# Kernel optimization log

Hardware: AMD Instinct MI355X
Metric: run time of the kernel (lower is better)

The kernel has to match this reference:

```python
import jax, jax.numpy as jnp
import numpy as np

EPS = 1e-6
NUM_HEADS = 12


def ln_cf(x, w, b):
    # channels_first LayerNorm over channel dim (ConvNeXt style)
    u = jnp.mean(x, axis=1, keepdims=True)
    s = jnp.mean((x - u) ** 2, axis=1, keepdims=True)
    xn = (x - u) / jnp.sqrt(s + EPS)
    shp = (1, -1) + (1,) * (x.ndim - 2)
    return xn * w.reshape(shp) + b.reshape(shp)


def conv2s2(x, w):
    # Conv3d kernel=2 stride=2 (no bias): exact non-overlapping patch contraction
    b, c, H, W, D = x.shape
    xp = x.reshape(b, c, H // 2, 2, W // 2, 2, D // 2, 2)
    return jnp.einsum('bchkwpdq,ockpq->bohwd', xp, w)


def convt2s2(x, w):
    # ConvTranspose3d kernel=2 stride=2 (torch weight layout [in, out, 2,2,2])
    b, i, H, W, D = x.shape
    o = w.shape[1]
    y = jnp.einsum('bihwd,iokpq->bohkwpdq', x, w)
    return y.reshape(b, o, 2 * H, 2 * W, 2 * D)


def stem(x, w1, g1, b1, w2, g2, b2):
    h = conv2s2(x, w1)
    h = jax.nn.gelu(ln_cf(h, g1, b1), approximate=False)
    h = conv2s2(h, w2)
    return ln_cf(h, g2, b2)


def debed(x, tw1, g, b, tw2, tb2):
    h = convt2s2(x, tw1)
    h = jax.nn.gelu(ln_cf(h, g, b), approximate=False)
    return convt2s2(h, tw2) + tb2.reshape(1, -1, 1, 1, 1)


def rope(x):
    # rotary embedding over full token dim c (pairs (i, i+c/2)), positions 0..L-1
    b, l, c = x.shape
    inv = 1.0 / (10000.0 ** (jnp.arange(0, c, 2, dtype=jnp.float32) / c))
    t = jnp.arange(l, dtype=jnp.float32)
    f = jnp.outer(t, inv)                      # [l, c/2]
    emb = jnp.concatenate([f, f], axis=-1)     # [l, c]
    cos, sin = jnp.cos(emb)[None], jnp.sin(emb)[None]
    rot = jnp.concatenate([-x[..., c // 2:], x[..., :c // 2]], axis=-1)
    return x * cos + rot * sin


def _forward(x, skip, q_w1, q_g1, q_b1, q_w2, q_g2, q_b2,
             k_w1, k_g1, k_b1, k_w2, k_g2, k_b2,
             v_w1, v_g1, v_b1, v_w2, v_g2, v_b2,
             o_tw1, o_g, o_b, o_tw2, o_tb2,
             ns_w, ns_b, nx_w, nx_b, no_w, no_b):
    res = skip
    skip = ln_cf(skip, ns_w, ns_b)
    x = ln_cf(x, nx_w, nx_b)
    q = stem(skip, q_w1, q_g1, q_b1, q_w2, q_g2, q_b2)
    k = stem(x, k_w1, k_g1, k_b1, k_w2, k_g2, k_b2)
    v = stem(x, v_w1, v_g1, v_b1, v_w2, v_g2, v_b2)
    b, c, Hq, Wq, Dq = q.shape
    _, _, Hk, Wk, Dk = k.shape
    q = q.reshape(b, c, -1).transpose(0, 2, 1)   # [b, Lq, c]
    k = k.reshape(b, c, -1).transpose(0, 2, 1)   # [b, Lk, c]
    v = v.reshape(b, c, -1).transpose(0, 2, 1)
    q = rope(q)
    k = rope(k)
    hd = c // NUM_HEADS
    qh = q.reshape(b, -1, NUM_HEADS, hd).transpose(0, 2, 1, 3)  # [b, nh, Lq, hd]
    kh = k.reshape(b, -1, NUM_HEADS, hd).transpose(0, 2, 1, 3)
    vh = v.reshape(b, -1, NUM_HEADS, hd).transpose(0, 2, 1, 3)
    scale = 1.0 / jnp.sqrt(jnp.float32(hd))
    attn = jax.nn.softmax(jnp.einsum('bhqc,bhkc->bhqk', qh, kh) * scale, axis=-1)
    proj = jnp.einsum('bhqk,bhkc->bhqc', attn, vh)              # [b, nh, Lq, hd]
    # rearrange 'b nh l c -> b (c nh) h w d'
    proj = proj.transpose(0, 3, 1, 2).reshape(b, c, Hq, Wq, Dq)
    proj = ln_cf(proj, no_w, no_b)
    out = debed(proj, o_tw1, o_g, o_b, o_tw2, o_tb2)
    return out + res


def setup_inputs() -> dict:
    key = jax.random.key(0)
    ks = iter(jax.random.split(key, 40))
    def nrm(shape, scale):
        return jax.random.normal(next(ks), shape, jnp.float32) * scale
    E, E4, XF, SF = 768, 192, 6, 6
    inp = {
        'x': nrm((2, XF, 48, 48, 48), 1.0),
        'skip': nrm((2, SF, 48, 48, 48), 1.0),
    }
    for p, ic in [('q', SF), ('k', XF), ('v', XF)]:
        inp[p + '_w1'] = nrm((E4, ic, 2, 2, 2), (ic * 8) ** -0.5)
        inp[p + '_g1'] = jnp.ones(E4, jnp.float32)
        inp[p + '_b1'] = jnp.zeros(E4, jnp.float32)
        inp[p + '_w2'] = nrm((E, E4, 2, 2, 2), (E4 * 8) ** -0.5)
        inp[p + '_g2'] = jnp.ones(E, jnp.float32)
        inp[p + '_b2'] = jnp.zeros(E, jnp.float32)
    inp['o_tw1'] = nrm((E, E4, 2, 2, 2), E ** -0.5)
    inp['o_g'] = jnp.ones(E4, jnp.float32)
    inp['o_b'] = jnp.zeros(E4, jnp.float32)
    inp['o_tw2'] = nrm((E4, SF, 2, 2, 2), E4 ** -0.5)
    inp['o_tb2'] = jnp.zeros(SF, jnp.float32)
    inp['ns_w'] = jnp.ones(SF, jnp.float32)
    inp['ns_b'] = jnp.zeros(SF, jnp.float32)
    inp['nx_w'] = jnp.ones(XF, jnp.float32)
    inp['nx_b'] = jnp.zeros(XF, jnp.float32)
    inp['no_w'] = jnp.ones(E, jnp.float32)
    inp['no_b'] = jnp.zeros(E, jnp.float32)
    return inp


def reference(x, skip, q_w1, q_g1, q_b1, q_w2, q_g2, q_b2,
              k_w1, k_g1, k_b1, k_w2, k_g2, k_b2,
              v_w1, v_g1, v_b1, v_w2, v_g2, v_b2,
              o_tw1, o_g, o_b, o_tw2, o_tb2,
              ns_w, ns_b, nx_w, nx_b, no_w, no_b):
    return _forward(x, skip, q_w1, q_g1, q_b1, q_w2, q_g2, q_b2,
                    k_w1, k_g1, k_b1, k_w2, k_g2, k_b2,
                    v_w1, v_g1, v_b1, v_w2, v_g2, v_b2,
                    o_tw1, o_g, o_b, o_tw2, o_tb2,
                    ns_w, ns_b, nx_w, nx_b, no_w, no_b)
```

## Files before the change

### kernel.cpp

```cpp
#include <hip/hip_runtime.h>
#include <math.h>

#define BB_ 2
#define C0 6
#define S0 48
#define V0 (S0*S0*S0)
#define C1 192
#define S1 24
#define V1 (S1*S1*S1)
#define C2 768
#define S2 12
#define LL (S2*S2*S2)
#define NH 12
#define HD 64
#define KDIM (C1*8)
#define MDIM (BB_*LL)

typedef __attribute__((ext_vector_type(8))) short short8;
typedef __attribute__((ext_vector_type(4))) short short4v;
typedef __attribute__((ext_vector_type(4))) float float4v;

static __device__ __forceinline__ float gelu_exact(float x){
  return 0.5f*x*(1.0f+erff(x*0.70710678118654752440f));
}
static __device__ __forceinline__ unsigned short f2bf(float f){
  unsigned int u = __float_as_uint(f);
  unsigned int r = (u + 0x7fffu + ((u>>16)&1u)) >> 16;
  return (unsigned short)r;
}
static __device__ __forceinline__ unsigned int pk_bf16(float a, float b){
#if __has_builtin(__builtin_amdgcn_cvt_pk_bf16_f32)
  typedef __attribute__((ext_vector_type(2))) __bf16 bf2;
  bf2 r = __builtin_amdgcn_cvt_pk_bf16_f32(a,b);
  union { bf2 v; unsigned int u; } cv; cv.v = r;
  return cv.u;
#else
  return (unsigned int)f2bf(a) | ((unsigned int)f2bf(b)<<16);
#endif
}
static __device__ __forceinline__ float bf2f(unsigned short u){
  return __uint_as_float(((unsigned int)u)<<16);
}
static __device__ __forceinline__ void load_lds16(const void* g, void* l){
  __builtin_amdgcn_global_load_lds((const __attribute__((address_space(1))) unsigned int*)g,
      (__attribute__((address_space(3))) unsigned int*)l, 16, 0, 0);
}
static __device__ __forceinline__ float4v mfma32(short8 a, short8 b, float4v c){
  return __builtin_amdgcn_mfma_f32_16x16x32_bf16(a,b,c,0,0,0);
}
static __device__ __forceinline__ float4v mfma16(short4v a, short4v b, float4v c){
#if __has_builtin(__builtin_amdgcn_mfma_f32_16x16x16bf16_1k)
  return __builtin_amdgcn_mfma_f32_16x16x16bf16_1k(a,b,c,0,0,0);
#else
  asm volatile("v_mfma_f32_16x16x16_bf16 %0, %1, %2, %0" : "+v"(c) : "v"(a), "v"(b));
  return c;
#endif
}

__global__ __launch_bounds__(256) void prep_kernel(
    const float* __restrict__ skin, const float* __restrict__ xin,
    const float* __restrict__ nsw, const float* __restrict__ nsb,
    const float* __restrict__ nxw, const float* __restrict__ nxb,
    unsigned short* __restrict__ outS, unsigned short* __restrict__ outX,
    const float* __restrict__ qw2, const float* __restrict__ kw2, const float* __restrict__ vw2,
    const float* __restrict__ tw1, const float* __restrict__ tw2,
    const float* __restrict__ qw1, const float* __restrict__ kw1, const float* __restrict__ vw1,
    unsigned short* __restrict__ w2tq, unsigned short* __restrict__ w2tk,
    unsigned short* __restrict__ w2tv, unsigned short* __restrict__ Btd,
    unsigned short* __restrict__ Bt48,
    unsigned short* __restrict__ w1q, unsigned short* __restrict__ w1k,
    unsigned short* __restrict__ w1v){
  int bx = blockIdx.x;
  if (bx < 1728){
    int z = bx >= 864;
    const float* in = z ? xin : skin;
    const float* w  = z ? nxw : nsw;
    const float* bi = z ? nxb : nsb;
    unsigned short* out = z ? outX : outS;
    int idx = (bx - z*864)*256 + threadIdx.x;
    int b = idx / V0, vox = idx - b*V0;
    const float* p = in + (size_t)b*(C0*V0) + vox;
    float v[C0]; float s=0.f;
#pragma unroll
    for (int c=0;c<C0;c++){ v[c]=p[(size_t)c*V0]; s+=v[c]; }
    float u = s*(1.f/C0);
    float ss=0.f;
#pragma unroll
    for (int c=0;c<C0;c++){ float d=v[c]-u; ss+=d*d; }
    float inv = rsqrtf(ss*(1.f/C0)+1e-6f);
    unsigned short* o = out + (size_t)b*(C0*V0) + vox;
#pragma unroll
    for (int c=0;c<C0;c++) o[(size_t)c*V0] = f2bf((v[c]-u)*inv*w[c]+bi[c]);
    return;
  }
  bx -= 1728;
  if (bx < 13824){
    int z = bx/4608;
    int idx = (bx - z*4608)*256 + threadIdx.x;
    const float* w2 = (z==0)?qw2:((z==1)?kw2:vw2);
    unsigned short* o = (z==0)?w2tq:((z==1)?w2tk:w2tv);
    int oc = idx/KDIM; int r = idx-oc*KDIM; int p = r/C1; int ic = r-p*C1;
    o[idx] = f2bf(w2[(size_t)oc*KDIM + ic*8 + p]);
  } else if (bx < 18432){
    int idx = (bx-13824)*256 + threadIdx.x;
    int n = idx/C2; int p = idx-n*C2;
    int i = ((p&63)*NH) + (p>>6);
    int kpq = n/C1, o2 = n-kpq*C1;
    Btd[idx] = f2bf(tw1[(size_t)i*KDIM + o2*8 + kpq]);
  } else if (bx < 18480){
    int idx = (bx-18432)*256 + threadIdx.x;
    int n = idx/C1; int i = idx-n*C1;
    Bt48[idx] = (n<48) ? f2bf(tw2[(size_t)i*48 + n]) : (unsigned short)0;
  } else {
    int idx = (bx-18480)*256 + threadIdx.x;
    int z = idx / 9216; int r = idx - z*9216;
    const float* w1 = (z==0)?qw1:((z==1)?kw1:vw1);
    unsigned short* o = (z==0)?w1q:((z==1)?w1k:w1v);
    o[r] = f2bf(w1[r]);
  }
}

__global__ __launch_bounds__(256) void conv1_kernel(
    const unsigned short* __restrict__ lnSb, const unsigned short* __restrict__ lnXb,
    const unsigned short* __restrict__ w1bq, const unsigned short* __restrict__ w1bk,
    const unsigned short* __restrict__ w1bv,
    const float* __restrict__ qg1, const float* __restrict__ qb1,
    const float* __restrict__ kg1, const float* __restrict__ kb1,
    const float* __restrict__ vg1, const float* __restrict__ vb1,
    unsigned short* __restrict__ h1q, unsigned short* __restrict__ h1k,
    unsigned short* __restrict__ h1v){
  int z = blockIdx.z;
  const unsigned short* in = (z==0)? lnSb : lnXb;
  const unsigned short* Wb = (z==0)?w1bq:((z==1)?w1bk:w1bv);
  const float* g1 = (z==0)?qg1:((z==1)?kg1:vg1);
  const float* b1 = (z==0)?qb1:((z==1)?kb1:vb1);
  unsigned short* h1p = (z==0)?h1q:((z==1)?h1k:h1v);
  int t = threadIdx.x, w = t>>6, lane = t&63;
  int g = lane>>4, l16 = lane&15;
  int j = blockIdx.x*4 + w;
  int bxh = j/18, mt = j - bxh*18;
  int b = bxh/48; int rem = bxh - b*48; int y = rem>>1, xh = rem&1;
  int xo = mt/3, zo = mt - xo*3;
  int xv = xh*12 + xo*2 + (l16>>3);
  int zv = zo*8 + (l16&7);
  int x2 = 2*xv, z2 = 2*zv, y2 = 2*y;
  const unsigned short* base = in + (size_t)b*C0*V0;
  union { short8 v; unsigned int u[4]; } aA;
  {
    size_t rb = (size_t)g*V0;
    aA.u[0] = *(const unsigned int*)&base[rb + (y2+0)*(S0*S0) + (x2+0)*S0 + z2];
    aA.u[1] = *(const unsigned int*)&base[rb + (y2+0)*(S0*S0) + (x2+1)*S0 + z2];
    aA.u[2] = *(const unsigned int*)&base[rb + (y2+1)*(S0*S0) + (x2+0)*S0 + z2];
    aA.u[3] = *(const unsigned int*)&base[rb + (y2+1)*(S0*S0) + (x2+1)*S0 + z2];
  }
  union { short4v v; unsigned int u[2]; } aB;
  {
    size_t rb = (size_t)(4+(g>>1))*V0 + (y2+(g&1))*(S0*S0);
    aB.u[0] = *(const unsigned int*)&base[rb + (x2+0)*S0 + z2];
    aB.u[1] = *(const unsigned int*)&base[rb + (x2+1)*S0 + z2];
  }
  float4v acc[12];
#pragma unroll
  for (int ot=0; ot<12; ot++){
    short8  wA = *(const short8*)&Wb[(ot*16+l16)*48 + g*8];
    short4v wB = *(const short4v*)&Wb[(ot*16+l16)*48 + 32 + g*4];
    float4v a = {};
    a = mfma32(wA, aA.v, a);
    a = mfma16(wB, aB.v, a);
    acc[ot] = a;
  }
  float s1=0.f, s2=0.f;
#pragma unroll
  for (int ot=0;ot<12;ot++)
#pragma unroll
    for (int reg=0;reg<4;reg++){ float v=acc[ot][reg]; s1+=v; s2+=v*v; }
  s1 += __shfl_xor(s1,16); s1 += __shfl_xor(s1,32);
  s2 += __shfl_xor(s2,16); s2 += __shfl_xor(s2,32);
  float u = s1*(1.f/C1);
  float inv = rsqrtf(s2*(1.f/C1)-u*u+1e-6f);
  int tok = (y>>1)*(S2*S2) + (xv>>1)*S2 + (zv>>1);
  int p8 = (y&1)*4 + (xv&1)*2 + (zv&1);
  unsigned short* hb = h1p + (size_t)(b*LL+tok)*KDIM + p8*C1;
#pragma unroll
  for (int ot=0; ot<12; ot++){
    int oc0 = ot*16 + g*4;
    float4 gg = *(const float4*)&g1[oc0];
    float4 bb = *(const float4*)&b1[oc0];
    float x0 = gelu_exact((acc[ot][0]-u)*inv*gg.x+bb.x);
    float x1 = gelu_exact((acc[ot][1]-u)*inv*gg.y+bb.y);
    float x2e= gelu_exact((acc[ot][2]-u)*inv*gg.z+bb.z);
    float x3 = gelu_exact((acc[ot][3]-u)*inv*gg.w+bb.w);
    uint2 pk; pk.x = pk_bf16(x0,x1); pk.y = pk_bf16(x2e,x3);
    *(uint2*)&hb[oc0] = pk;
  }
}

__global__ __launch_bounds__(256) void gemm_stem_kernel(
    const unsigned short* __restrict__ A0, const unsigned short* __restrict__ A1,
    const unsigned short* __restrict__ A2,
    const unsigned short* __restrict__ B0, const unsigned short* __restrict__ B1,
    const unsigned short* __restrict__ B2,
    unsigned short* __restrict__ Cq, unsigned short* __restrict__ Ck,
    unsigned short* __restrict__ Cv){
  int flat = blockIdx.x;
  int xcd = flat & 7, slot = flat >> 3;
  int tile = xcd*61 + slot;
  if (tile >= 486) return;
  int z = tile/162; int rr = tile - z*162;
  int m0 = (rr/6)*128, n0 = (rr - (rr/6)*6)*128;
  const unsigned short* A = (z==0)?A0:((z==1)?A1:A2);
  const unsigned short* Bt = (z==0)?B0:((z==1)?B1:B2);
  unsigned short* Cp = (z==0)?Cq:((z==1)?Ck:Cv);
  __shared__ __align__(16) unsigned short Al[128*32];
  __shared__ __align__(16) unsigned short Bl[128*32];
  int t=threadIdx.x, w=t>>6, lane=t&63;
  int g=lane>>4, l16=lane&15, r16=lane>>2, c16=lane&3;
  int wm=w>>1, wn=w&1;
  float4v acc[4][4] = {};
  for (int kb=0;kb<KDIM;kb+=32){
    __syncthreads();
#pragma unroll
    for (int cc=0;cc<4;cc++){
      int ch = w*4+cc;
      if (ch<8){
        const unsigned short* gp = A + (size_t)(m0+ch*16+r16)*KDIM + kb + c16*8;
        load_lds16(gp, &Al[ch*512]);
      } else {
        const unsigned short* gp = Bt + (size_t)(n0+(ch-8)*16+r16)*KDIM + kb + c16*8;
        load_lds16(gp, &Bl[(ch-8)*512]);
      }
    }
    __syncthreads();
    short8 af[4], bf[4];
#pragma unroll
    for (int mt=0;mt<4;mt++) af[mt] = *(const short8*)&Al[(wm*64+mt*16+l16)*32 + g*8];
#pragma unroll
    for (int nt=0;nt<4;nt++) bf[nt] = *(const short8*)&Bl[(wn*64+nt*16+l16)*32 + g*8];
#pragma unroll
    for (int mt=0;mt<4;mt++)
#pragma unroll
      for (int nt=0;nt<4;nt++)
        acc[mt][nt] = mfma32(af[mt], bf[nt], acc[mt][nt]);
  }
#pragma unroll
  for (int mt=0;mt<4;mt++){
    int mb = m0 + wm*64 + mt*16 + g*4;
#pragma unroll
    for (int nt=0;nt<4;nt++){
      int col = n0 + wn*64 + nt*16 + l16;
#pragma unroll
      for (int reg=0;reg<4;reg++)
        Cp[(size_t)(mb+reg)*C2 + col] = f2bf(acc[mt][nt][reg]);
    }
  }
}

__global__ __launch_bounds__(256) void gemm_debed_kernel(const unsigned short* __restrict__ A,
    const unsigned short* __restrict__ Bt, unsigned short* __restrict__ C){
  int flat = blockIdx.x;
  int xcd = flat & 7, slot = flat >> 3;
  int tile = xcd*41 + slot;
  if (tile >= 324) return;
  int m0 = (tile/12)*128, n0 = (tile - (tile/12)*12)*128;
  __shared__ __align__(16) unsigned short Al[128*32];
  __shared__ __align__(16) unsigned short Bl[128*32];
  int t=threadIdx.x, w=t>>6, lane=t&63;
  int g=lane>>4, l16=lane&15, r16=lane>>2, c16=lane&3;
  int wm=w>>1, wn=w&1;
  float4v acc[4][4] = {};
  for (int kb=0;kb<C2;kb+=32){
    __syncthreads();
#pragma unroll
    for (int cc=0;cc<4;cc++){
      int ch = w*4+cc;
      if (ch<8){
        const unsigned short* gp = A + (size_t)(m0+ch*16+r16)*C2 + kb + c16*8;
        load_lds16(gp, &Al[ch*512]);
      } else {
        const unsigned short* gp = Bt + (size_t)(n0+(ch-8)*16+r16)*C2 + kb + c16*8;
        load_lds16(gp, &Bl[(ch-8)*512]);
      }
    }
    __syncthreads();
    short8 af[4], bf[4];
#pragma unroll
    for (int mt=0;mt<4;mt++) af[mt] = *(const short8*)&Al[(wm*64+mt*16+l16)*32 + g*8];
#pragma unroll
    for (int nt=0;nt<4;nt++) bf[nt] = *(const short8*)&Bl[(wn*64+nt*16+l16)*32 + g*8];
#pragma unroll
    for (int mt=0;mt<4;mt++)
#pragma unroll
      for (int nt=0;nt<4;nt++)
        acc[mt][nt] = mfma32(af[mt], bf[nt], acc[mt][nt]);
  }
#pragma unroll
  for (int nt=0;nt<4;nt++){
    int n = n0 + wn*64 + nt*16 + l16;
    int kpq = n / C1;
    int o = n - kpq*C1;
#pragma unroll
    for (int mt=0;mt<4;mt++){
      int mb = m0 + wm*64 + mt*16 + g*4;
#pragma unroll
      for (int reg=0;reg<4;reg++){
        int m = mb + reg;
        int b = m / LL; int tok = m - b*LL;
        int h = tok/(S2*S2), ww=(tok/S2)%S2, d=tok%S2;
        int v24 = (2*h+((kpq>>2)&1))*(S1*S1) + (2*ww+((kpq>>1)&1))*S1 + (2*d+(kpq&1));
        C[(size_t)(b*V1+v24)*C1 + o] = f2bf(acc[mt][nt][reg]);
      }
    }
  }
}

__global__ __launch_bounds__(256) void final_kernel(const unsigned short* __restrict__ dh,
    const unsigned short* __restrict__ Bt48, const float* __restrict__ og,
    const float* __restrict__ ob, const float* __restrict__ tb2s,
    const float* __restrict__ skipp, float* __restrict__ out){
  __shared__ __align__(16) unsigned short As[64*200];
  __shared__ __align__(16) unsigned short Bs[64*200];
  int t=threadIdx.x, w=t>>6, lane=t&63;
  int g=lane>>4, l16=lane&15;
  int m0 = blockIdx.x*64;
  for (int n8 = t; n8 < 1536; n8 += 256){
    int n64 = n8/24, kk = (n8 - n64*24)*8;
    uint4 d4 = *(const uint4*)&Bt48[n64*192 + kk];
    *(uint4*)&Bs[n64*200 + kk] = d4;
  }
  float g0=og[lane], g1v=og[lane+64], g2v=og[lane+128];
  float b0=ob[lane], b1v=ob[lane+64], b2v=ob[lane+128];
  for (int rr=0; rr<16; rr++){
    int rl = w*16 + rr;
    const unsigned short* row = dh + (size_t)(m0+rl)*C1;
    float v0=bf2f(row[lane]), v1=bf2f(row[lane+64]), v2=bf2f(row[lane+128]);
    float s1=v0+v1+v2, s2=v0*v0+v1*v1+v2*v2;
#pragma unroll
    for (int off=32;off>0;off>>=1){ s1+=__shfl_xor(s1,off); s2+=__shfl_xor(s2,off); }
    float u=s1*(1.f/C1), inv=rsqrtf(s2*(1.f/C1)-u*u+1e-6f);
    As[rl*200+lane]     = f2bf(gelu_exact((v0-u)*inv*g0+b0));
    As[rl*200+lane+64]  = f2bf(gelu_exact((v1-u)*inv*g1v+b1v));
    As[rl*200+lane+128] = f2bf(gelu_exact((v2-u)*inv*g2v+b2v));
  }
  __syncthreads();
  int wm=w>>1, wn=w&1;
  float4v acc[2][2] = {};
#pragma unroll
  for (int kb=0;kb<192;kb+=32){
    short8 af[2], bf[2];
#pragma unroll
    for (int mt=0;mt<2;mt++) af[mt] = *(const short8*)&As[(wm*32+mt*16+l16)*200 + kb + g*8];
#pragma unroll
    for (int nt=0;nt<2;nt++) bf[nt] = *(const short8*)&Bs[(wn*32+nt*16+l16)*200 + kb + g*8];
#pragma unroll
    for (int mt=0;mt<2;mt++)
#pragma unroll
      for (int nt=0;nt<2;nt++)
        acc[mt][nt] = mfma32(af[mt], bf[nt], acc[mt][nt]);
  }
#pragma unroll
  for (int nt=0;nt<2;nt++){
    int n = wn*32 + nt*16 + l16;
    if (n < 48){
      int c = n>>3, kpq = n&7;
      float bias = tb2s[c];
#pragma unroll
      for (int mt=0;mt<2;mt++){
        int mb = m0 + wm*32 + mt*16 + g*4;
#pragma unroll
        for (int reg=0;reg<4;reg++){
          int m = mb + reg;
          int b = m / V1; int v24 = m - b*V1;
          int y24 = v24/(S1*S1), x24=(v24/S1)%S1, z24=v24%S1;
          int vox = (2*y24+((kpq>>2)&1))*(S0*S0) + (2*x24+((kpq>>1)&1))*S0 + 2*z24+(kpq&1);
          size_t oi = (size_t)(b*C0+c)*V0 + vox;
          out[oi] = acc[mt][nt][reg] + bias + skipp[oi];
        }
      }
    }
  }
}

__global__ __launch_bounds__(64) void ln768_stem_kernel(
    unsigned short* __restrict__ qb, unsigned short* __restrict__ kb2,
    unsigned short* __restrict__ vb,
    const float* __restrict__ qg, const float* __restrict__ qbi,
    const float* __restrict__ kg, const float* __restrict__ kbi,
    const float* __restrict__ vg, const float* __restrict__ vbi, float qscale){
  int z = blockIdx.y;
  unsigned short* buf = (z==0)?qb:((z==1)?kb2:vb);
  const float* g  = (z==0)?qg:((z==1)?kg:vg);
  const float* bia= (z==0)?qbi:((z==1)?kbi:vbi);
  float scale = (z==0)? qscale : 1.0f;
  int tok = blockIdx.x, lane = threadIdx.x;
  unsigned short* row = buf + (size_t)tok*C2;
  float v[12]; float s1=0.f,s2=0.f;
#pragma unroll
  for (int i=0;i<12;i++){ float t=bf2f(row[i*64+lane]); v[i]=t; s1+=t; s2+=t*t; }
#pragma unroll
  for (int off=32;off>0;off>>=1){ s1+=__shfl_xor(s1,off); s2+=__shfl_xor(s2,off); }
  float u=s1*(1.f/C2);
  float inv=rsqrtf(s2*(1.f/C2)-u*u+1e-6f);
  if (z==2){
#pragma unroll
    for (int i=0;i<12;i++){ int j=i*64+lane; row[j]=f2bf((v[i]-u)*inv*g[j]+bia[j]); }
  } else {
    int pos = tok % LL;
#pragma unroll
    for (int i=0;i<6;i++){
      int j=i*64+lane;
      float xn1=(v[i]-u)*inv*g[j]+bia[j];
      float xn2=(v[i+6]-u)*inv*g[j+384]+bia[j+384];
      float fr=(float)pos*__expf(-0.02398526139f*(float)j);
      float cs=cosf(fr), sn=sinf(fr);
      row[j]     = f2bf((xn1*cs - xn2*sn)*scale);
      row[j+384] = f2bf((xn2*cs + xn1*sn)*scale);
    }
  }
}

__global__ __launch_bounds__(256) void vtrans_kernel(const unsigned short* __restrict__ vbf,
    unsigned short* __restrict__ vT){
  __shared__ unsigned short T[64*72];
  int tok0 = blockIdx.x*64;
  int h = blockIdx.y, b = blockIdx.z;
  int t = threadIdx.x;
#pragma unroll
  for (int i=0;i<2;i++){
    int idx = t + i*256;
    int token = idx>>3, dc = idx&7;
    uint4 d4 = *(const uint4*)&vbf[(size_t)(b*LL+tok0+token)*C2 + h*64 + dc*8];
    const unsigned short* s = (const unsigned short*)&d4;
#pragma unroll
    for (int j2=0;j2<8;j2++) T[(dc*8+j2)*72 + token] = s[j2];
  }
  __syncthreads();
  int r = t>>2, seg = t&3;
  unsigned short* dst = vT + (size_t)((b*NH+h)*HD + r)*LL + tok0 + seg*16;
  uint4 o[2];
  unsigned short* os = (unsigned short*)o;
#pragma unroll
  for (int j2=0;j2<16;j2++) os[j2] = T[r*72 + seg*16 + j2];
  *(uint4*)dst = o[0];
  *(uint4*)(dst+8) = o[1];
}

__global__ __launch_bounds__(256) void attn_kernel(const unsigned short* __restrict__ q,
    const unsigned short* __restrict__ k, const unsigned short* __restrict__ vt,
    unsigned short* __restrict__ opart, float* __restrict__ lbuf){
  __shared__ __align__(16) unsigned char smem[18432];
  unsigned short* Ks = (unsigned short*)smem;
  unsigned short* Vs = Ks + 4096;
  int flat = blockIdx.x;
  int xcd = flat & 7, slot = flat >> 3;
  int tile = xcd*324 + slot;
  int h = tile / 216; int rem = tile - h*216;
  int zb = rem / 27, qt = rem - zb*27;
  int b = zb >> 2, split = zb & 3;
  int t=threadIdx.x, w=t>>6, lane=t&63;
  int g=lane>>4, l16=lane&15;
  const unsigned short* qrow = q + (size_t)(b*LL + qt*64 + w*16 + l16)*C2 + h*64;
  short8 qA = *(const short8*)(qrow + g*8);
  short8 qB = *(const short8*)(qrow + 32 + g*8);
  const unsigned short* kbase = k + (size_t)(b*LL)*C2 + h*64;
  const unsigned short* vbase = vt + (size_t)((b*NH+h)*HD)*LL;
  int sub = lane>>3;
  int chs = (lane&7) ^ sub;
  int ktb = split*7, kte = (split==3)? 27 : (split*7+7);
  const unsigned short* gptr[4];
  unsigned short* ldst[4];
  int gstep[4];
#pragma unroll
  for (int cc=0;cc<4;cc++){
    int ii = w*4+cc;
    if (ii<8){
      int key = ktb*64 + ii*8 + sub;
      gptr[cc] = kbase + (size_t)key*C2 + chs*8;
      gstep[cc] = 64*C2;
      ldst[cc] = &Ks[ii*512];
    } else {
      int d = (ii-8)*8 + sub;
      gptr[cc] = vbase + (size_t)d*LL + ktb*64 + chs*8;
      gstep[cc] = 64;
      ldst[cc] = &Vs[(ii-8)*512];
    }
  }
  int sw = l16 & 7;
  const unsigned short* ksrow = &Ks[l16*64 + (g^sw)*8];
  int c2d = (((4+g)^sw) - (g^sw))*8;
  const unsigned short* vsrow = &Vs[l16*64 + (g&1)*4];
  int xk[4];
#pragma unroll
  for (int kc=0;kc<4;kc++) xk[kc] = (((kc*2 + (g>>1)) ^ sw))*8;
  short4v vones;
  vones[0]=vones[1]=vones[2]=vones[3]=(short)0x3F80;
  float4v O4[4] = {};
  float4v Ol = {};
  for (int kt=ktb; kt<kte; kt++){
    __syncthreads();
#pragma unroll
    for (int cc=0;cc<4;cc++){
      load_lds16(gptr[cc], ldst[cc]);
      gptr[cc] += gstep[cc];
    }
    __syncthreads();
    float4v sc[4];
#pragma unroll
    for (int nt=0;nt<4;nt++){
      short8 k1 = *(const short8*)(ksrow + nt*1024);
      short8 k2 = *(const short8*)(ksrow + nt*1024 + c2d);
      float4v z = {};
      z = mfma32(k1, qA, z);
      z = mfma32(k2, qB, z);
      sc[nt] = z;
    }
#pragma unroll
    for (int nt=0;nt<4;nt++)
#pragma unroll
      for (int reg=0;reg<4;reg++)
        sc[nt][reg] = exp2f(sc[nt][reg]);
#pragma unroll
    for (int kc=0;kc<4;kc++){
      union { short4v v; unsigned int u[2]; } pb;
      pb.u[0] = pk_bf16(sc[kc][0], sc[kc][1]);
      pb.u[1] = pk_bf16(sc[kc][2], sc[kc][3]);
      Ol = mfma16(vones, pb.v, Ol);
      const unsigned short* vp = vsrow + xk[kc];
#pragma unroll
      for (int dt=0;dt<4;dt++){
        short4v va = *(const short4v*)(vp + dt*1024);
        O4[dt] = mfma16(va, pb.v, O4[dt]);
      }
    }
  }
  __syncthreads();
  float* Ot = (float*)smem;
  float* ot = Ot + w*1152;
#pragma unroll
  for (int dt=0;dt<4;dt++)
    *(float4*)&ot[l16*72 + dt*16 + g*4] =
        make_float4(O4[dt][0],O4[dt][1],O4[dt][2],O4[dt][3]);
  if (g==0){
    int qi = qt*64 + w*16 + l16;
    lbuf[((size_t)(b*4+split)*NH+h)*LL + qi] = Ol[0];
  }
  int qq = lane>>2, c4 = lane&3;
  unsigned short* orow = opart + (size_t)split*MDIM*C2
              + (size_t)(b*LL + qt*64 + w*16 + qq)*C2 + h*64;
#pragma unroll
  for (int p=0;p<4;p++){
    float4 vv = *(float4*)&ot[qq*72 + p*16 + c4*4];
    uint2 pk; pk.x = pk_bf16(vv.x,vv.y); pk.y = pk_bf16(vv.z,vv.w);
    *(uint2*)&orow[p*16 + c4*4] = pk;
  }
}

__global__ __launch_bounds__(256) void attn_post_kernel(const unsigned short* __restrict__ opart,
    const float* __restrict__ lbuf,
    const float* __restrict__ g, const float* __restrict__ bia,
    unsigned short* __restrict__ aob){
  int t=threadIdx.x, w=t>>6, lane=t&63;
  int m = blockIdx.x*4 + w;
  int b = m / LL, l = m - b*LL;
  const unsigned short* o0 = opart + (size_t)m*C2;
  unsigned short* orow = aob + (size_t)m*C2;
  float vv[12]; float s1=0.f, s2=0.f;
#pragma unroll
  for (int i=0;i<12;i++){
    float ls = 0.f;
#pragma unroll
    for (int s=0;s<4;s++) ls += lbuf[((size_t)(b*4+s)*NH+i)*LL + l];
    float inv = 1.f/ls;
    int j = i*64+lane;
    float val = 0.f;
#pragma unroll
    for (int s=0;s<4;s++) val += bf2f(o0[(size_t)s*MDIM*C2 + j]);
    val *= inv;
    vv[i]=val; s1+=val; s2+=val*val;
  }
#pragma unroll
  for (int off=32;off>0;off>>=1){ s1+=__shfl_xor(s1,off); s2+=__shfl_xor(s2,off); }
  float u=s1*(1.f/C2);
  float invs=rsqrtf(s2*(1.f/C2)-u*u+1e-6f);
#pragma unroll
  for (int i=0;i<12;i++){
    int cj = lane*NH + i;
    orow[i*64+lane] = f2bf((vv[i]-u)*invs*g[cj]+bia[cj]);
  }
}

extern "C" void kernel_launch(void* const* d_in, const int* in_sizes, int n_in,
                              void* d_out, int out_size, void* d_ws, size_t ws_size,
                              hipStream_t stream){
  (void)in_sizes; (void)n_in; (void)out_size; (void)ws_size;
  const float* x    =(const float*)d_in[0];
  const float* skip =(const float*)d_in[1];
  const float* q_w1 =(const float*)d_in[2];
  const float* q_g1 =(const float*)d_in[3];
  const float* q_b1 =(const float*)d_in[4];
  const float* q_w2 =(const float*)d_in[5];
  const float* q_g2 =(const float*)d_in[6];
  const float* q_b2 =(const float*)d_in[7];
  const float* k_w1 =(const float*)d_in[8];
  const float* k_g1 =(const float*)d_in[9];
  const float* k_b1 =(const float*)d_in[10];
  const float* k_w2 =(const float*)d_in[11];
  const float* k_g2 =(const float*)d_in[12];
  const float* k_b2 =(const float*)d_in[13];
  const float* v_w1 =(const float*)d_in[14];
  const float* v_g1 =(const float*)d_in[15];
  const float* v_b1 =(const float*)d_in[16];
  const float* v_w2 =(const float*)d_in[17];
  const float* v_g2 =(const float*)d_in[18];
  const float* v_b2 =(const float*)d_in[19];
  const float* o_tw1=(const float*)d_in[20];
  const float* o_g  =(const float*)d_in[21];
  const float* o_b  =(const float*)d_in[22];
  const float* o_tw2=(const float*)d_in[23];
  const float* o_tb2=(const float*)d_in[24];
  const float* ns_w =(const float*)d_in[25];
  const float* ns_b =(const float*)d_in[26];
  const float* nx_w =(const float*)d_in[27];
  const float* nx_b =(const float*)d_in[28];
  const float* no_w =(const float*)d_in[29];
  const float* no_b =(const float*)d_in[30];
  float* out=(float*)d_out;

  char* W = (char*)d_ws;
  unsigned short* lnSb = (unsigned short*)(W + 0);
  unsigned short* lnXb = (unsigned short*)(W + 2654208);
  unsigned short* h1q  = (unsigned short*)(W + 5308416);
  unsigned short* h1k  = (unsigned short*)(W + 15925248);
  unsigned short* h1v  = (unsigned short*)(W + 26542080);
  unsigned short* w2tq = (unsigned short*)(W + 37158912);
  unsigned short* w2tk = (unsigned short*)(W + 39518208);
  unsigned short* w2tv = (unsigned short*)(W + 41877504);
  unsigned short* qbf  = (unsigned short*)(W + 44236800);
  unsigned short* kbf  = (unsigned short*)(W + 49545216);
  unsigned short* vbf  = (unsigned short*)(W + 54853632);
  unsigned short* vT   = (unsigned short*)(W + 60162048);
  unsigned short* aob  = (unsigned short*)(W + 65470464);
  unsigned short* Btd  = (unsigned short*)(W + 70778880);
  unsigned short* Bt48 = (unsigned short*)(W + 73138176);
  unsigned short* w1q  = (unsigned short*)(W + 73162752);
  unsigned short* w1k  = (unsigned short*)(W + 73181184);
  unsigned short* w1v  = (unsigned short*)(W + 73199616);
  float* lbuf  = (float*)(W + 0);
  unsigned short* opart = (unsigned short*)(W + 5308416);
  unsigned short* dh   = (unsigned short*)(W + 5308416);

  const float QSCALE = 0.125f*1.44269504089f;

  prep_kernel<<<20316,256,0,stream>>>(skip, x, ns_w, ns_b, nx_w, nx_b, lnSb, lnXb,
      q_w2,k_w2,v_w2,o_tw1,o_tw2, q_w1,k_w1,v_w1,
      w2tq,w2tk,w2tv,Btd,Bt48, w1q,w1k,w1v);
  conv1_kernel<<<dim3(432,1,3),256,0,stream>>>(lnSb,lnXb, w1q,w1k,w1v,
      q_g1,q_b1, k_g1,k_b1, v_g1,v_b1, h1q,h1k,h1v);
  gemm_stem_kernel<<<488,256,0,stream>>>(h1q,h1k,h1v,
      w2tq,w2tk,w2tv, qbf,kbf,vbf);
  ln768_stem_kernel<<<dim3(MDIM,3),64,0,stream>>>(qbf,kbf,vbf,
      q_g2,q_b2, k_g2,k_b2, v_g2,v_b2, QSCALE);
  vtrans_kernel<<<dim3(27,12,2),256,0,stream>>>(vbf, vT);
  attn_kernel<<<2592,256,0,stream>>>(qbf, kbf, vT, opart, lbuf);
  attn_post_kernel<<<864,256,0,stream>>>(opart, lbuf, no_w, no_b, aob);
  gemm_debed_kernel<<<328,256,0,stream>>>(aob, Btd, dh);
  final_kernel<<<432,256,0,stream>>>(dh, Bt48, o_g, o_b, o_tb2, skip, out);
}
```

Baseline: 330.5 us.

## Double-buffer LDS tiles in stem/debed GEMMs and attention loop

Converts the shared-memory tiles in the stem GEMM, debed GEMM and attention kernels to double buffers, so the next K/V or A/B tile is loaded while the current one is consumed. This removes one barrier per iteration and overlaps global-to-LDS loads with MFMA work. Shared-memory use per block roughly doubles, which may lower occupancy. The attention epilogue also changes its output staging stride from 72 to 76 and adds a barrier before the cross-lane read-back.

```diff
diff --git a/kernel.cpp b/kernel.cpp
--- a/kernel.cpp
+++ b/kernel.cpp
@@ -211,36 +211,52 @@
   const unsigned short* A = (z==0)?A0:((z==1)?A1:A2);
   const unsigned short* Bt = (z==0)?B0:((z==1)?B1:B2);
   unsigned short* Cp = (z==0)?Cq:((z==1)?Ck:Cv);
-  __shared__ __align__(16) unsigned short Al[128*32];
-  __shared__ __align__(16) unsigned short Bl[128*32];
+  __shared__ __align__(16) unsigned short Al[2][128*32];
+  __shared__ __align__(16) unsigned short Bl[2][128*32];
   int t=threadIdx.x, w=t>>6, lane=t&63;
   int g=lane>>4, l16=lane&15, r16=lane>>2, c16=lane&3;
   int wm=w>>1, wn=w&1;
   float4v acc[4][4] = {};
+#pragma unroll
+  for (int cc=0;cc<4;cc++){
+    int ch = w*4+cc;
+    if (ch<8){
+      const unsigned short* gp = A + (size_t)(m0+ch*16+r16)*KDIM + 0 + c16*8;
+      load_lds16(gp, &Al[0][ch*512]);
+    } else {
+      const unsigned short* gp = Bt + (size_t)(n0+(ch-8)*16+r16)*KDIM + 0 + c16*8;
+      load_lds16(gp, &Bl[0][(ch-8)*512]);
+    }
+  }
+  __syncthreads();
+  int cur = 0;
   for (int kb=0;kb<KDIM;kb+=32){
-    __syncthreads();
-#pragma unroll
-    for (int cc=0;cc<4;cc++){
-      int ch = w*4+cc;
-      if (ch<8){
-        const unsigned short* gp = A + (size_t)(m0+ch*16+r16)*KDIM + kb + c16*8;
-        load_lds16(gp, &Al[ch*512]);
-      } else {
-        const unsigned short* gp = Bt + (size_t)(n0+(ch-8)*16+r16)*KDIM + kb + c16*8;
-        load_lds16(gp, &Bl[(ch-8)*512]);
+    if (kb+32 < KDIM){
+      int nb = cur^1;
+#pragma unroll
+      for (int cc=0;cc<4;cc++){
+        int ch = w*4+cc;
+        if (ch<8){
+          const unsigned short* gp = A + (size_t)(m0+ch*16+r16)*KDIM + (kb+32) + c16*8;
+          load_lds16(gp, &Al[nb][ch*512]);
+        } else {
+          const unsigned short* gp = Bt + (size_t)(n0+(ch-8)*16+r16)*KDIM + (kb+32) + c16*8;
+          load_lds16(gp, &Bl[nb][(ch-8)*512]);
+        }
       }
     }
-    __syncthreads();
     short8 af[4], bf[4];
 #pragma unroll
-    for (int mt=0;mt<4;mt++) af[mt] = *(const short8*)&Al[(wm*64+mt*16+l16)*32 + g*8];
-#pragma unroll
-    for (int nt=0;nt<4;nt++) bf[nt] = *(const short8*)&Bl[(wn*64+nt*16+l16)*32 + g*8];
+    for (int mt=0;mt<4;mt++) af[mt] = *(const short8*)&Al[cur][(wm*64+mt*16+l16)*32 + g*8];
+#pragma unroll
+    for (int nt=0;nt<4;nt++) bf[nt] = *(const short8*)&Bl[cur][(wn*64+nt*16+l16)*32 + g*8];
 #pragma unroll
     for (int mt=0;mt<4;mt++)
 #pragma unroll
       for (int nt=0;nt<4;nt++)
         acc[mt][nt] = mfma32(af[mt], bf[nt], acc[mt][nt]);
+    __syncthreads();
+    cur ^= 1;
   }
 #pragma unroll
   for (int mt=0;mt<4;mt++){
@@ -262,36 +278,52 @@
   int tile = xcd*41 + slot;
   if (tile >= 324) return;
   int m0 = (tile/12)*128, n0 = (tile - (tile/12)*12)*128;
-  __shared__ __align__(16) unsigned short Al[128*32];
-  __shared__ __align__(16) unsigned short Bl[128*32];
+  __shared__ __align__(16) unsigned short Al[2][128*32];
+  __shared__ __align__(16) unsigned short Bl[2][128*32];
   int t=threadIdx.x, w=t>>6, lane=t&63;
   int g=lane>>4, l16=lane&15, r16=lane>>2, c16=lane&3;
   int wm=w>>1, wn=w&1;
   float4v acc[4][4] = {};
+#pragma unroll
+  for (int cc=0;cc<4;cc++){
+    int ch = w*4+cc;
+    if (ch<8){
+      const unsigned short* gp = A + (size_t)(m0+ch*16+r16)*C2 + 0 + c16*8;
+      load_lds16(gp, &Al[0][ch*512]);
+    } else {
+      const unsigned short* gp = Bt + (size_t)(n0+(ch-8)*16+r16)*C2 + 0 + c16*8;
+      load_lds16(gp, &Bl[0][(ch-8)*512]);
+    }
+  }
+  __syncthreads();
+  int cur = 0;
   for (int kb=0;kb<C2;kb+=32){
-    __syncthreads();
-#pragma unroll
-    for (int cc=0;cc<4;cc++){
-      int ch = w*4+cc;
-      if (ch<8){
-        const unsigned short* gp = A + (size_t)(m0+ch*16+r16)*C2 + kb + c16*8;
-        load_lds16(gp, &Al[ch*512]);
-      } else {
-        const unsigned short* gp = Bt + (size_t)(n0+(ch-8)*16+r16)*C2 + kb + c16*8;
-        load_lds16(gp, &Bl[(ch-8)*512]);
+    if (kb+32 < C2){
+      int nb = cur^1;
+#pragma unroll
+      for (int cc=0;cc<4;cc++){
+        int ch = w*4+cc;
+        if (ch<8){
+          const unsigned short* gp = A + (size_t)(m0+ch*16+r16)*C2 + (kb+32) + c16*8;
+          load_lds16(gp, &Al[nb][ch*512]);
+        } else {
+          const unsigned short* gp = Bt + (size_t)(n0+(ch-8)*16+r16)*C2 + (kb+32) + c16*8;
+          load_lds16(gp, &Bl[nb][(ch-8)*512]);
+        }
       }
     }
-    __syncthreads();
     short8 af[4], bf[4];
 #pragma unroll
-    for (int mt=0;mt<4;mt++) af[mt] = *(const short8*)&Al[(wm*64+mt*16+l16)*32 + g*8];
-#pragma unroll
-    for (int nt=0;nt<4;nt++) bf[nt] = *(const short8*)&Bl[(wn*64+nt*16+l16)*32 + g*8];
+    for (int mt=0;mt<4;mt++) af[mt] = *(const short8*)&Al[cur][(wm*64+mt*16+l16)*32 + g*8];
+#pragma unroll
+    for (int nt=0;nt<4;nt++) bf[nt] = *(const short8*)&Bl[cur][(wn*64+nt*16+l16)*32 + g*8];
 #pragma unroll
     for (int mt=0;mt<4;mt++)
 #pragma unroll
       for (int nt=0;nt<4;nt++)
         acc[mt][nt] = mfma32(af[mt], bf[nt], acc[mt][nt]);
+    __syncthreads();
+    cur ^= 1;
   }
 #pragma unroll
   for (int nt=0;nt<4;nt++){
@@ -447,7 +479,7 @@
 __global__ __launch_bounds__(256) void attn_kernel(const unsigned short* __restrict__ q,
     const unsigned short* __restrict__ k, const unsigned short* __restrict__ vt,
     unsigned short* __restrict__ opart, float* __restrict__ lbuf){
-  __shared__ __align__(16) unsigned char smem[18432];
+  __shared__ __align__(16) unsigned char smem[32768];
   unsigned short* Ks = (unsigned short*)smem;
   unsigned short* Vs = Ks + 4096;
   int flat = blockIdx.x;
@@ -495,23 +527,34 @@
   vones[0]=vones[1]=vones[2]=vones[3]=(short)0x3F80;
   float4v O4[4] = {};
   float4v Ol = {};
+#pragma unroll
+  for (int cc=0;cc<4;cc++){
+    load_lds16(gptr[cc], ldst[cc]);
+    gptr[cc] += gstep[cc];
+  }
+  __syncthreads();
+  int cur = 0;
   for (int kt=ktb; kt<kte; kt++){
-    __syncthreads();
-#pragma unroll
-    for (int cc=0;cc<4;cc++){
-      load_lds16(gptr[cc], ldst[cc]);
-      gptr[cc] += gstep[cc];
-    }
-    __syncthreads();
+    if (kt+1 < kte){
+      int so = (cur^1)*8192;
+#pragma unroll
+      for (int cc=0;cc<4;cc++){
+        load_lds16(gptr[cc], ldst[cc]+so);
+        gptr[cc] += gstep[cc];
+      }
+    }
+    int co = cur*8192;
+    const unsigned short* kr = ksrow + co;
+    const unsigned short* vr = vsrow + co;
     float4v sc[4];
 #pragma unroll
     for (int nt=0;nt<4;nt++){
-      short8 k1 = *(const short8*)(ksrow + nt*1024);
-      short8 k2 = *(const short8*)(ksrow + nt*1024 + c2d);
-      float4v z = {};
-      z = mfma32(k1, qA, z);
-      z = mfma32(k2, qB, z);
-      sc[nt] = z;
+      short8 k1 = *(const short8*)(kr + nt*1024);
+      short8 k2 = *(const short8*)(kr + nt*1024 + c2d);
+      float4v zz = {};
+      zz = mfma32(k1, qA, zz);
+      zz = mfma32(k2, qB, zz);
+      sc[nt] = zz;
     }
 #pragma unroll
     for (int nt=0;nt<4;nt++)
@@ -524,31 +567,33 @@
       pb.u[0] = pk_bf16(sc[kc][0], sc[kc][1]);
       pb.u[1] = pk_bf16(sc[kc][2], sc[kc][3]);
       Ol = mfma16(vones, pb.v, Ol);
-      const unsigned short* vp = vsrow + xk[kc];
+      const unsigned short* vp = vr + xk[kc];
 #pragma unroll
       for (int dt=0;dt<4;dt++){
         short4v va = *(const short4v*)(vp + dt*1024);
         O4[dt] = mfma16(va, pb.v, O4[dt]);
       }
     }
-  }
-  __syncthreads();
+    __syncthreads();
+    cur ^= 1;
+  }
   float* Ot = (float*)smem;
-  float* ot = Ot + w*1152;
+  float* ot = Ot + w*1216;
 #pragma unroll
   for (int dt=0;dt<4;dt++)
-    *(float4*)&ot[l16*72 + dt*16 + g*4] =
+    *(float4*)&ot[l16*76 + dt*16 + g*4] =
         make_float4(O4[dt][0],O4[dt][1],O4[dt][2],O4[dt][3]);
   if (g==0){
     int qi = qt*64 + w*16 + l16;
     lbuf[((size_t)(b*4+split)*NH+h)*LL + qi] = Ol[0];
   }
+  __syncthreads();
   int qq = lane>>2, c4 = lane&3;
   unsigned short* orow = opart + (size_t)split*MDIM*C2
               + (size_t)(b*LL + qt*64 + w*16 + qq)*C2 + h*64;
 #pragma unroll
   for (int p=0;p<4;p++){
-    float4 vv = *(float4*)&ot[qq*72 + p*16 + c4*4];
+    float4 vv = *(float4*)&ot[qq*76 + p*16 + c4*4];
     uint2 pk; pk.x = pk_bf16(vv.x,vv.y); pk.y = pk_bf16(vv.z,vv.w);
     *(uint2*)&orow[p*16 + c4*4] = pk;
   }
```

Result: no change. 325.3 us (-1.6%).
